# Kernel optimization log

Measured on AMD Instinct MI355X. Metric: run time of the kernel, lower is better.

Reference implementation:

```python
import jax, jax.numpy as jnp
import numpy as np
from jax import lax

N = 5000            # number of detections
FEAT = 1024         # last-layer feature dim; 1024 + 9 engineered feats = indim 1033
DIMS = [FEAT + 9, 1000, 600, 300, 150, 1]
IOU_THRESH = 0.5
EPS = 2.220446049250313e-16  # sys.float_info.epsilon


def setup_inputs() -> dict:
    key = jax.random.key(0)
    ks = jax.random.split(key, 8 + 3 * len(DIMS))
    H, W = 800.0, 1333.0
    cx = jax.random.uniform(ks[0], (N,), minval=0.0, maxval=W)
    cy = jax.random.uniform(ks[1], (N,), minval=0.0, maxval=H)
    bw = jax.random.uniform(ks[2], (N,), minval=20.0, maxval=250.0)
    bh = jax.random.uniform(ks[3], (N,), minval=20.0, maxval=250.0)
    x1 = jnp.clip(cx - bw / 2, 0.0, W - 2)
    y1 = jnp.clip(cy - bh / 2, 0.0, H - 2)
    x2 = jnp.clip(cx + bw / 2, x1 + 1, W)
    y2 = jnp.clip(cy + bh / 2, y1 + 1, H)
    inp = {
        'multi_bboxes': jnp.stack([x1, y1, x2, y2], axis=1),
        'cls_score': jax.random.uniform(ks[4], (N, 2)),
        'last_layer_feats': jax.random.normal(ks[5], (N, FEAT)),
        'img_shape': jnp.array([H, W], jnp.float32),
    }
    # PermEqui2_mean params: Gamma (weight+bias) and Lambda (weight only)
    ki = 6
    for i, (din, dout) in enumerate(zip(DIMS[:-1], DIMS[1:])):
        s = 1.0 / np.sqrt(din)
        inp[f'Wg{i+1}'] = jax.random.uniform(ks[ki], (dout, din), minval=-s, maxval=s); ki += 1
        inp[f'bg{i+1}'] = jax.random.uniform(ks[ki], (dout,), minval=-s, maxval=s); ki += 1
        inp[f'Wl{i+1}'] = jax.random.uniform(ks[ki], (dout, din), minval=-s, maxval=s); ki += 1
    return inp


def _greedy_cluster(ious, thresh):
    # Sequential greedy IoU clustering (NMS-like). assign[i] = index of cluster seed.
    n = ious.shape[0]

    def step(carry, inp):
        is_c, assign = carry
        j, row = inp
        seed = is_c[j]
        hit = row > thresh
        member = seed & hit & is_c
        assign = jnp.where(member, j, assign)
        is_c = is_c & ~(seed & hit)
        return (is_c, assign), None

    init = (jnp.ones(n, bool), jnp.zeros(n, jnp.int32))
    (_, assign), _ = lax.scan(step, init, (jnp.arange(n, dtype=jnp.int32), ious))
    return assign


def _forward(multi_bboxes, cls_score, last_layer_feats, img_shape, params):
    n = multi_bboxes.shape[0]
    scores = cls_score[:, 1]
    order = jnp.argsort(-scores)
    scores = scores[order]
    bboxes = multi_bboxes[order]
    feats = last_layer_feats[order]

    x1, y1, x2, y2 = bboxes[:, 0], bboxes[:, 1], bboxes[:, 2], bboxes[:, 3]
    # pairwise IoU with the +1 pixel convention from bbox_overlaps
    iw = jnp.clip(jnp.minimum(x2[:, None], x2[None, :]) - jnp.maximum(x1[:, None], x1[None, :]) + 1, 0)
    ih = jnp.clip(jnp.minimum(y2[:, None], y2[None, :]) - jnp.maximum(y1[:, None], y1[None, :]) + 1, 0)
    area = (x2 - x1 + 1) * (y2 - y1 + 1)
    overlap = iw * ih
    ious = overlap / (area[:, None] + area[None, :] - overlap)

    assign = _greedy_cluster(lax.stop_gradient(ious), IOU_THRESH)
    counts = jax.ops.segment_sum(jnp.ones(n, jnp.float32), assign, num_segments=n)
    cden = jnp.maximum(counts, 1.0)

    Himg, Wimg = img_shape[0], img_shape[1]
    # source double-normalizes: width = (x2/W - x1/W)/W, height = (y2/H - y1/H)/H
    width = (x2 / Wimg - x1 / Wimg) / Wimg
    height = (y2 / Himg - y1 / Himg) / Himg
    areaf = width * height
    ar = width / (height + EPS)
    x = jnp.concatenate([
        bboxes, feats,
        width[:, None], height[:, None], ar[:, None], areaf[:, None], scores[:, None],
    ], axis=1)  # [n, 1033]

    def perm_equi(x, Wg, bg, Wl):
        # xm = per-set mean; x*Gamma^T + b - (xm*Lambda^T), gathered back per box
        xm = jax.ops.segment_sum(x, assign, num_segments=n) / cden[:, None]
        return x @ Wg.T + bg - (xm @ Wl.T)[assign]

    for i in range(5):
        x = jax.nn.elu(perm_equi(x, params[f'Wg{i+1}'], params[f'bg{i+1}'], params[f'Wl{i+1}']))

    # source skips singleton sets (nonzero().squeeze() -> 0-dim): mask them out
    valid = counts[assign] >= 2.0
    return jnp.where(valid[:, None], x, 0.0)  # [n, 1] per-box set logits


def reference(multi_bboxes, cls_score, last_layer_feats, img_shape,
              Wg1, bg1, Wl1, Wg2, bg2, Wl2, Wg3, bg3, Wl3,
              Wg4, bg4, Wl4, Wg5, bg5, Wl5):
    params = {'Wg1': Wg1, 'bg1': bg1, 'Wl1': Wl1, 'Wg2': Wg2, 'bg2': bg2, 'Wl2': Wl2,
              'Wg3': Wg3, 'bg3': bg3, 'Wl3': Wl3, 'Wg4': Wg4, 'bg4': bg4, 'Wl4': Wl4,
              'Wg5': Wg5, 'bg5': bg5, 'Wl5': Wl5}
    return _forward(multi_bboxes, cls_score, last_layer_feats, img_shape, params)
```

## Files before the change

### kernel.cpp

```cpp
#include <hip/hip_runtime.h>
#include <cstdint>
#include <cstddef>

#define N_BOX 5000
#define NW    80
#define LDX   1040
#define LDZ   2048
#define LDYM  1000
#define LDW   1040
#define LDAB  2080
#define NCHUNK ((N_BOX + 63) / 64)
#define RT    ((N_BOX + 255) / 256)

typedef short bf16x8 __attribute__((ext_vector_type(8)));
typedef float f32x4v __attribute__((ext_vector_type(4)));
typedef unsigned short u16x8 __attribute__((ext_vector_type(8)));

__device__ __forceinline__ float fence_f(float x) { asm volatile("" : "+v"(x)); return x; }

__device__ __forceinline__ unsigned short f2bf(float x) {
    unsigned u = __builtin_bit_cast(unsigned, x);
    unsigned r = (u + 0x7FFFu + ((u >> 16) & 1u)) >> 16;
    return (unsigned short)r;
}
__device__ __forceinline__ float bf2f(unsigned short h) {
    unsigned u = ((unsigned)h) << 16;
    return __builtin_bit_cast(float, u);
}

__global__ void rank_partial_kernel(const float* __restrict__ cls, int* __restrict__ rank) {
    __shared__ float sj[256];
    int t = threadIdx.x;
    int jbase = blockIdx.y * 256;
    int jg = jbase + t;
    sj[t] = (jg < N_BOX) ? cls[2 * jg + 1] : 0.0f;
    __syncthreads();
    int i = blockIdx.x * 256 + t;
    if (i >= N_BOX) return;
    float si = cls[2 * i + 1];
    int jmax = (N_BOX - jbase < 256) ? (N_BOX - jbase) : 256;
    int r = 0;
    for (int k = 0; k < jmax; ++k) {
        float sjv = sj[k];
        int j = jbase + k;
        r += (sjv > si) || (sjv == si && j < i);
    }
    atomicAdd(&rank[i], r);
}

__global__ void rank_scatter_kernel(const int* __restrict__ rank, int* __restrict__ ord) {
    int i = blockIdx.x * blockDim.x + threadIdx.x;
    if (i < N_BOX) ord[rank[i]] = i;
}

__global__ void gather_kernel(const float* __restrict__ bb, const float* __restrict__ cls,
                              const float* __restrict__ feats, const float* __restrict__ img,
                              const int* __restrict__ ord,
                              float* __restrict__ X0, float* __restrict__ sb) {
    int r = blockIdx.x;
    int i = ord[r];
    float x1 = bb[4 * i + 0], y1 = bb[4 * i + 1], x2 = bb[4 * i + 2], y2 = bb[4 * i + 3];
    float H = img[0], W = img[1];
    float sc = cls[2 * i + 1];
    if (threadIdx.x == 0) {
        sb[0 * N_BOX + r] = x1;
        sb[1 * N_BOX + r] = y1;
        sb[2 * N_BOX + r] = x2;
        sb[3 * N_BOX + r] = y2;
        sb[4 * N_BOX + r] = (x2 - x1 + 1.0f) * (y2 - y1 + 1.0f);
        sb[5 * N_BOX + r] = sc;
    }
    float width  = (x2 / W - x1 / W) / W;
    float height = (y2 / H - y1 / H) / H;
    float ar     = width / (height + 2.220446049250313e-16f);
    float areaf  = width * height;
    float* row = X0 + (size_t)r * LDX;
    for (int o = threadIdx.x; o < LDX; o += blockDim.x) {
        float v;
        if (o < 4)          v = (o == 0) ? x1 : (o == 1) ? y1 : (o == 2) ? x2 : y2;
        else if (o < 1028)  v = feats[(size_t)i * 1024 + (o - 4)];
        else if (o == 1028) v = width;
        else if (o == 1029) v = height;
        else if (o == 1030) v = ar;
        else if (o == 1031) v = areaf;
        else if (o == 1032) v = sc;
        else                v = 0.0f;
        row[o] = v;
    }
}

__global__ void mask_kernel(const float* __restrict__ sb, unsigned long long* __restrict__ mask,
                            unsigned long long* __restrict__ diag) {
    int j = blockIdx.x;
    const float* X1 = sb;
    const float* Y1 = sb + N_BOX;
    const float* X2 = sb + 2 * N_BOX;
    const float* Y2 = sb + 3 * N_BOX;
    const float* AR = sb + 4 * N_BOX;
    float xj1 = X1[j], yj1 = Y1[j], xj2 = X2[j], yj2 = Y2[j], aj = AR[j];
    int lane = threadIdx.x & 63;
    int wave = threadIdx.x >> 6;
    int nwav = blockDim.x >> 6;
    int dw = j >> 6;
    for (int w = wave; w < NW; w += nwav) {
        int i = w * 64 + lane;
        bool pred = false;
        if (i < N_BOX) {
            float iw = fmaxf(fminf(xj2, X2[i]) - fmaxf(xj1, X1[i]) + 1.0f, 0.0f);
            float ih = fmaxf(fminf(yj2, Y2[i]) - fmaxf(yj1, Y1[i]) + 1.0f, 0.0f);
            float ov = fence_f(iw * ih);
            float denom = fence_f((aj + AR[i]) - ov);
            pred = (ov / denom) > 0.5f;
        }
        unsigned long long b = __ballot(pred);
        if (lane == 0) {
            mask[(size_t)j * NW + w] = b;
            if (w == dw) diag[j] = b;
        }
    }
}

__device__ __forceinline__ void nms_body(const unsigned long long* __restrict__ mask,
                                         const unsigned long long* __restrict__ diag,
                                         unsigned long long* __restrict__ keep,
                                         unsigned long long* supp,
                                         unsigned long long* keep_sh,
                                         unsigned long long* rem_sh,
                                         unsigned long long* kb_sh) {
    int tid = threadIdx.x;
    int l = tid & 63;
    int w = tid >> 6;
    if (tid < 80) supp[tid] = 0ULL;
    unsigned long long dg = 0ULL, dg_next = 0ULL;
    if (w == 0) dg = diag[l];
    __syncthreads();
    for (int c = 0; c < NCHUNK; ++c) {
        if (w == 0) {
            unsigned long long curv = supp[c];
            unsigned clo = __builtin_amdgcn_readfirstlane((unsigned)curv);
            unsigned chi = __builtin_amdgcn_readfirstlane((unsigned)(curv >> 32));
            unsigned long long cur = ((unsigned long long)chi << 32) | clo;
            int jmax = (N_BOX - c * 64 < 64) ? (N_BOX - c * 64) : 64;
            unsigned long long valid = (jmax >= 64) ? ~0ULL : ((1ULL << jmax) - 1ULL);
            unsigned long long rem = ~cur & valid;
            if (l == 0) *rem_sh = rem;
        }
        __syncthreads();
        unsigned long long rem0 = *rem_sh;
        unsigned long long a0 = 0, a1 = 0, a2 = 0, a3 = 0, a4 = 0;
        unsigned long long b0 = 0, b1 = 0, b2 = 0, b3 = 0, b4 = 0;
        unsigned mym = 0;
        int base = (w - 1) * 5;
        if (w > 0) {
            mym = (base < 64) ? (unsigned)((rem0 >> base) & 31ULL) : 0u;
            const unsigned long long* rowp = mask + (size_t)(c * 64 + base) * NW;
            if (mym & 1u)  { a0 = rowp[0 * NW + l]; b0 = (l < 16) ? rowp[0 * NW + 64 + l] : 0ULL; }
            if (mym & 2u)  { a1 = rowp[1 * NW + l]; b1 = (l < 16) ? rowp[1 * NW + 64 + l] : 0ULL; }
            if (mym & 4u)  { a2 = rowp[2 * NW + l]; b2 = (l < 16) ? rowp[2 * NW + 64 + l] : 0ULL; }
            if (mym & 8u)  { a3 = rowp[3 * NW + l]; b3 = (l < 16) ? rowp[3 * NW + 64 + l] : 0ULL; }
            if (mym & 16u) { a4 = rowp[4 * NW + l]; b4 = (l < 16) ? rowp[4 * NW + 64 + l] : 0ULL; }
        } else {
            if (c + 1 < NCHUNK) dg_next = diag[(size_t)(c + 1) * 64 + l];
            unsigned rlo = __builtin_amdgcn_readfirstlane((unsigned)rem0);
            unsigned rhi = __builtin_amdgcn_readfirstlane((unsigned)(rem0 >> 32));
            unsigned long long remS = ((unsigned long long)rhi << 32) | rlo;
            unsigned long long kb = 0ULL;
            while (remS) {
                int jj = __builtin_ctzll(remS);
                kb |= 1ULL << jj;
                unsigned dlo = __builtin_amdgcn_readlane((unsigned)dg, jj);
                unsigned dhi = __builtin_amdgcn_readlane((unsigned)(dg >> 32), jj);
                unsigned long long dj = ((unsigned long long)dhi << 32) | dlo;
                remS &= ~dj;
                remS &= ~(1ULL << jj);
            }
            if (l == 0) { *kb_sh = kb; keep_sh[c] = kb; }
        }
        __syncthreads();
        if (w > 0 && mym) {
            unsigned long long kb = *kb_sh;
            unsigned kw = ((unsigned)((kb >> base) & 31ULL)) & mym;
            if (kw & 1u)  { atomicOr(&supp[l], a0); if (l < 16) atomicOr(&supp[64 + l], b0); }
            if (kw & 2u)  { atomicOr(&supp[l], a1); if (l < 16) atomicOr(&supp[64 + l], b1); }
            if (kw & 4u)  { atomicOr(&supp[l], a2); if (l < 16) atomicOr(&supp[64 + l], b2); }
            if (kw & 8u)  { atomicOr(&supp[l], a3); if (l < 16) atomicOr(&supp[64 + l], b3); }
            if (kw & 16u) { atomicOr(&supp[l], a4); if (l < 16) atomicOr(&supp[64 + l], b4); }
        }
        if (w == 0) dg = dg_next;
        __syncthreads();
    }
    if (tid < NCHUNK) keep[tid] = keep_sh[tid];
}

__global__ __launch_bounds__(1024) void nms_scan_kernel(const unsigned long long* __restrict__ mask,
                                                        const unsigned long long* __restrict__ diag,
                                                        unsigned long long* __restrict__ keep) {
    __shared__ unsigned long long supp[80];
    __shared__ unsigned long long keep_sh[NCHUNK];
    __shared__ unsigned long long rem_sh;
    __shared__ unsigned long long kb_sh;
    nms_body(mask, diag, keep, supp, keep_sh, &rem_sh, &kb_sh);
}

__global__ __launch_bounds__(1024) void nms_gemm_fused(const unsigned long long* __restrict__ mask,
                                                       const unsigned long long* __restrict__ diag,
                                                       unsigned long long* __restrict__ keep,
                                                       const unsigned short* __restrict__ A2,
                                                       const unsigned short* __restrict__ B2,
                                                       float* __restrict__ C, int KT, int Nn,
                                                       int MTiles) {
    __shared__ __align__(16) unsigned short AsBuf[2 * 8192];
    __shared__ __align__(16) unsigned short BsBuf[2 * 8192];
    int tid = threadIdx.x;
    if (blockIdx.x == 0) {
        unsigned long long* supp    = (unsigned long long*)AsBuf;
        unsigned long long* keep_sh = supp + 80;
        unsigned long long* rem_sh  = keep_sh + NCHUNK;
        unsigned long long* kb_sh   = rem_sh + 1;
        nms_body(mask, diag, keep, supp, keep_sh, rem_sh, kb_sh);
        return;
    }
    int t = blockIdx.x - 1;
    size_t bm = (size_t)(t % MTiles) * 256;
    size_t bn = (size_t)(t / MTiles) * 256;
    int lane = tid & 63;
    int wavef = tid >> 6;
    int wr = wavef >> 2, wc = wavef & 3;

    f32x4v acc[4][4];
#pragma unroll
    for (int i = 0; i < 4; ++i)
#pragma unroll
        for (int j = 0; j < 4; ++j) acc[i][j] = (f32x4v){0.f, 0.f, 0.f, 0.f};

    const unsigned short* gA = A2 + (bm + wavef * 16 + (lane & 15)) * (size_t)LDAB + (lane >> 4) * 8;
    const unsigned short* gB = B2 + (bn + wavef * 16 + (lane & 15)) * (size_t)LDAB + (lane >> 4) * 8;
    unsigned ldsoff = (unsigned)((wavef * 64 + lane) * 16);

#define FSTAGE(T, BUF)                                                                             \
    {                                                                                              \
        size_t ko = (size_t)(T) * 32;                                                              \
        __builtin_amdgcn_global_load_lds(                                                          \
            (const __attribute__((address_space(1))) void*)(gA + ko),                              \
            (__attribute__((address_space(3))) void*)((char*)AsBuf + (BUF) * 16384 + ldsoff),      \
            16, 0, 0);                                                                             \
        __builtin_amdgcn_global_load_lds(                                                          \
            (const __attribute__((address_space(1))) void*)(gB + ko),                              \
            (__attribute__((address_space(3))) void*)((char*)BsBuf + (BUF) * 16384 + ldsoff),      \
            16, 0, 0);                                                                             \
    }

    FSTAGE(0, 0);
    for (int kt = 0; kt < KT; ++kt) {
        int cur = kt & 1;
        if (kt + 1 < KT) {
            FSTAGE(kt + 1, cur ^ 1);
            asm volatile("s_waitcnt vmcnt(2)" ::: "memory");
        } else {
            asm volatile("s_waitcnt vmcnt(0)" ::: "memory");
        }
        asm volatile("s_barrier" ::: "memory");
        bf16x8 af[4], bf[4];
#pragma unroll
        for (int f4 = 0; f4 < 4; ++f4) {
            af[f4] = *(const bf16x8*)((const char*)AsBuf + cur * 16384 + ((wr * 4 + f4) * 64 + lane) * 16);
            bf[f4] = *(const bf16x8*)((const char*)BsBuf + cur * 16384 + ((wc * 4 + f4) * 64 + lane) * 16);
        }
#pragma unroll
        for (int i = 0; i < 4; ++i)
#pragma unroll
            for (int j = 0; j < 4; ++j)
                acc[i][j] = __builtin_amdgcn_mfma_f32_16x16x32_bf16(af[i], bf[j], acc[i][j], 0, 0, 0);
        asm volatile("s_barrier" ::: "memory");
    }
#undef FSTAGE

#pragma unroll
    for (int i = 0; i < 4; ++i) {
        int r0 = (int)bm + wr * 64 + i * 16 + (lane >> 4) * 4;
#pragma unroll
        for (int j = 0; j < 4; ++j) {
            int col = (int)bn + wc * 64 + j * 16 + (lane & 15);
            if (col < Nn) {
#pragma unroll
                for (int e = 0; e < 4; ++e) {
                    int r = r0 + e;
                    if (r < N_BOX) C[(size_t)r * LDZ + col] = acc[i][j][e];
                }
            }
        }
    }
}

__global__ void zero_counts_kernel(int* __restrict__ counts) {
    int i = blockIdx.x * blockDim.x + threadIdx.x;
    if (i < N_BOX) counts[i] = 0;
}

__global__ void assign_kernel(const unsigned long long* __restrict__ mask,
                              const unsigned long long* __restrict__ keep,
                              int* __restrict__ assign, int* __restrict__ counts) {
    int i = blockIdx.x * blockDim.x + threadIdx.x;
    if (i >= N_BOX) return;
    for (int w = 0; w < NCHUNK; ++w) {
        unsigned long long m = mask[(size_t)i * NW + w] & keep[w];
        if (m) {
            int j = w * 64 + __builtin_ctzll(m);
            assign[i] = j;
            atomicAdd(&counts[j], 1);
            return;
        }
    }
}

__global__ __launch_bounds__(1024) void scan_kernel(const int* __restrict__ counts, int* __restrict__ offs) {
    __shared__ int part[1024];
    int t = threadIdx.x;
    int base = t * 5;
    int c[5];
    int s = 0;
#pragma unroll
    for (int k = 0; k < 5; ++k) {
        int idx = base + k;
        c[k] = (idx < N_BOX) ? counts[idx] : 0;
        s += c[k];
    }
    part[t] = s;
    __syncthreads();
    for (int d = 1; d < 1024; d <<= 1) {
        int v = part[t];
        int u = (t >= d) ? part[t - d] : 0;
        __syncthreads();
        part[t] = v + u;
        __syncthreads();
    }
    int run = (t > 0) ? part[t - 1] : 0;
#pragma unroll
    for (int k = 0; k < 5; ++k) {
        int idx = base + k;
        if (idx < N_BOX) offs[idx] = run;
        run += c[k];
    }
}

__global__ void rankscatter_kernel(const int* __restrict__ assign, const int* __restrict__ offs,
                                   int* __restrict__ members) {
    __shared__ int a[N_BOX];
    int tid = threadIdx.x;
    for (int t = tid; t < N_BOX; t += blockDim.x) a[t] = assign[t];
    __syncthreads();
    int i = blockIdx.x * blockDim.x + tid;
    if (i >= N_BOX) return;
    int ai = a[i];
    int r = 0;
    for (int k = 0; k < i; ++k) r += (a[k] == ai);
    members[offs[ai] + r] = i;
}

__global__ void xconv_kernel(const float* __restrict__ X, unsigned short* __restrict__ A2,
                             int K16eff, int colOff) {
    int r = blockIdx.x;
    unsigned short* dst = A2 + (size_t)r * LDAB;
    int K2 = 2 * K16eff;
    int nk8 = K2 >> 3;
    if (r >= N_BOX) {
        for (int k8 = threadIdx.x; k8 < nk8; k8 += blockDim.x) {
            u16x8 z;
#pragma unroll
            for (int j = 0; j < 8; ++j) z[j] = 0;
            *(u16x8*)(dst + (k8 << 3)) = z;
        }
        return;
    }
    const float* src = X + (size_t)r * LDX + colOff;
    for (int k8 = threadIdx.x; k8 < nk8; k8 += blockDim.x) {
        int kb = k8 << 3;
        bool lo = (kb >= K16eff);
        int ks = lo ? (kb - K16eff) : kb;
        u16x8 out;
#pragma unroll
        for (int j = 0; j < 8; ++j) {
            float x = src[ks + j];
            unsigned short ah = f2bf(x);
            out[j] = lo ? f2bf(x - bf2f(ah)) : ah;
        }
        *(u16x8*)(dst + kb) = out;
    }
}

__global__ void wconv_kernel(const float* __restrict__ Wg, const float* __restrict__ Wl,
                             unsigned short* __restrict__ B2, int dout, int din_src,
                             int din_eff, int colOff, int K16eff) {
    int n = blockIdx.x;
    unsigned short* dst = B2 + (size_t)n * LDAB;
    int K2 = 2 * K16eff;
    if (n >= 2 * dout) {
        for (int k = threadIdx.x; k < K2; k += blockDim.x) dst[k] = 0;
        return;
    }
    const float* src = (n < dout) ? (Wg + (size_t)n * din_src) : (Wl + (size_t)(n - dout) * din_src);
    for (int k = threadIdx.x; k < K2; k += blockDim.x) {
        int ks = (k >= K16eff) ? (k - K16eff) : k;
        float x = (ks < din_eff) ? src[colOff + ks] : 0.0f;
        dst[k] = f2bf(x);
    }
}

__global__ void e9_kernel(const float* __restrict__ X0, float* __restrict__ E9) {
    int r = blockIdx.x * blockDim.x + threadIdx.x;
    if (r >= 5120) return;
    const int cq[9] = {0, 1, 2, 3, 1028, 1029, 1030, 1031, 1032};
    float* dst = E9 + (size_t)r * 12;
#pragma unroll
    for (int q = 0; q < 9; ++q) dst[q] = (r < N_BOX) ? X0[(size_t)r * LDX + cq[q]] : 0.0f;
    dst[9] = dst[10] = dst[11] = 0.0f;
}
__global__ void w9_kernel(const float* __restrict__ Wg, const float* __restrict__ Wl,
                          float* __restrict__ W9, int NB) {
    int n = blockIdx.x * blockDim.x + threadIdx.x;
    if (n >= NB) return;
    const int cq[9] = {0, 1, 2, 3, 1028, 1029, 1030, 1031, 1032};
    float* dst = W9 + (size_t)n * 12;
    const float* src = (n < 1000) ? (Wg + (size_t)n * 1033)
                     : (n < 2000) ? (Wl + (size_t)(n - 1000) * 1033) : nullptr;
#pragma unroll
    for (int q = 0; q < 9; ++q) dst[q] = src ? src[cq[q]] : 0.0f;
    dst[9] = dst[10] = dst[11] = 0.0f;
}

__global__ void z9_patch_kernel(float* __restrict__ Z, const float* __restrict__ E9,
                                const float* __restrict__ W9, int Nn) {
    int r = blockIdx.x;
    float e[9];
#pragma unroll
    for (int q = 0; q < 9; ++q) e[q] = E9[(size_t)r * 12 + q];
    for (int o = threadIdx.x; o < Nn; o += blockDim.x) {
        const float* w = W9 + (size_t)o * 12;
        float s = 0.0f;
#pragma unroll
        for (int q = 0; q < 9; ++q) s += e[q] * w[q];
        Z[(size_t)r * LDZ + o] += s;
    }
}

__global__ __launch_bounds__(256, 4) void gemm_mfma(const unsigned short* __restrict__ A2,
                                                    const unsigned short* __restrict__ B2,
                                                    float* __restrict__ C, int KT, int Nn) {
    __shared__ unsigned short AsBuf[2 * 4096];
    __shared__ unsigned short BsBuf[2 * 4096];
    int tid = threadIdx.x;
    int lane = tid & 63;
    int wave = tid >> 6;
    int wr = wave >> 1, wc = wave & 1;
    size_t bm = (size_t)blockIdx.x * 128;
    size_t bn = (size_t)blockIdx.y * 128;

    f32x4v acc[4][4];
#pragma unroll
    for (int i = 0; i < 4; ++i)
#pragma unroll
        for (int j = 0; j < 4; ++j) acc[i][j] = (f32x4v){0.f, 0.f, 0.f, 0.f};

    const unsigned short* gA[2];
    const unsigned short* gB[2];
    unsigned ldsoff[2];
#pragma unroll
    for (int q = 0; q < 2; ++q) {
        int f = q * 4 + wave;
        int grow = f * 16 + (lane & 15);
        int gcol = (lane >> 4) * 8;
        gA[q] = A2 + (bm + grow) * (size_t)LDAB + gcol;
        gB[q] = B2 + (bn + grow) * (size_t)LDAB + gcol;
        ldsoff[q] = (unsigned)((f * 64 + lane) * 16);
    }

#define STAGE(T, BUF)                                                                              \
    {                                                                                              \
        size_t ko = (size_t)(T) * 32;                                                              \
        _Pragma("unroll") for (int q = 0; q < 2; ++q) {                                            \
            __builtin_amdgcn_global_load_lds(                                                      \
                (const __attribute__((address_space(1))) void*)(gA[q] + ko),                       \
                (__attribute__((address_space(3))) void*)((char*)AsBuf + (BUF) * 8192 + ldsoff[q]),\
                16, 0, 0);                                                                         \
            __builtin_amdgcn_global_load_lds(                                                      \
                (const __attribute__((address_space(1))) void*)(gB[q] + ko),                       \
                (__attribute__((address_space(3))) void*)((char*)BsBuf + (BUF) * 8192 + ldsoff[q]),\
                16, 0, 0);                                                                         \
        }                                                                                          \
    }

    STAGE(0, 0);
    for (int kt = 0; kt < KT; ++kt) {
        int cur = kt & 1;
        if (kt + 1 < KT) {
            STAGE(kt + 1, cur ^ 1);
            asm volatile("s_waitcnt vmcnt(4)" ::: "memory");
        } else {
            asm volatile("s_waitcnt vmcnt(0)" ::: "memory");
        }
        asm volatile("s_barrier" ::: "memory");
        bf16x8 af[4], bf[4];
#pragma unroll
        for (int f4 = 0; f4 < 4; ++f4) {
            af[f4] = *(const bf16x8*)((const char*)AsBuf + cur * 8192 + ((wr * 4 + f4) * 64 + lane) * 16);
            bf[f4] = *(const bf16x8*)((const char*)BsBuf + cur * 8192 + ((wc * 4 + f4) * 64 + lane) * 16);
        }
#pragma unroll
        for (int i = 0; i < 4; ++i)
#pragma unroll
            for (int j = 0; j < 4; ++j)
                acc[i][j] = __builtin_amdgcn_mfma_f32_16x16x32_bf16(af[i], bf[j], acc[i][j], 0, 0, 0);
        asm volatile("s_barrier" ::: "memory");
    }
#undef STAGE

#pragma unroll
    for (int i = 0; i < 4; ++i) {
        int r0 = (int)bm + wr * 64 + i * 16 + (lane >> 4) * 4;
#pragma unroll
        for (int j = 0; j < 4; ++j) {
            int col = (int)bn + wc * 64 + j * 16 + (lane & 15);
            if (col < Nn) {
#pragma unroll
                for (int e = 0; e < 4; ++e) {
                    int r = r0 + e;
                    if (r < N_BOX) C[(size_t)r * LDZ + col] = acc[i][j][e];
                }
            }
        }
    }
}

__global__ void wcat_kernel(const float* __restrict__ Wg, const float* __restrict__ Wl,
                            float* __restrict__ Wc, int dout, int din, int K16) {
    int row = blockIdx.x;
    const float* src = (row < dout) ? (Wg + (size_t)row * din) : (Wl + (size_t)(row - dout) * din);
    float* dst = Wc + (size_t)row * LDW;
    for (int k = threadIdx.x; k < K16; k += blockDim.x)
        dst[k] = (k < din) ? src[k] : 0.0f;
}

__global__ __launch_bounds__(256) void gemm_nt(const float* __restrict__ A, const float* __restrict__ B,
                                               float* __restrict__ C, int M, int Nn, int K16) {
    __shared__ float As[16][64];
    __shared__ float Bs[16][64];
    int bm = blockIdx.x * 64;
    int bn = blockIdx.y * 64;
    int tid = threadIdx.x;
    int row = tid & 63;
    int kq  = tid >> 6;
    int tx  = tid & 15;
    int ty  = tid >> 4;
    float acc[4][4] = {};
    for (int k0 = 0; k0 < K16; k0 += 16) {
        float4 av = make_float4(0.f, 0.f, 0.f, 0.f);
        float4 bv = make_float4(0.f, 0.f, 0.f, 0.f);
        if (bm + row < M)  av = *(const float4*)&A[(size_t)(bm + row) * LDX + k0 + kq * 4];
        if (bn + row < Nn) bv = *(const float4*)&B[(size_t)(bn + row) * LDW + k0 + kq * 4];
        __syncthreads();
        As[kq * 4 + 0][row] = av.x; As[kq * 4 + 1][row] = av.y;
        As[kq * 4 + 2][row] = av.z; As[kq * 4 + 3][row] = av.w;
        Bs[kq * 4 + 0][row] = bv.x; Bs[kq * 4 + 1][row] = bv.y;
        Bs[kq * 4 + 2][row] = bv.z; Bs[kq * 4 + 3][row] = bv.w;
        __syncthreads();
#pragma unroll
        for (int kk = 0; kk < 16; ++kk) {
            float4 a = *(const float4*)&As[kk][ty * 4];
            float4 b = *(const float4*)&Bs[kk][tx * 4];
            float aa[4] = {a.x, a.y, a.z, a.w};
            float bb[4] = {b.x, b.y, b.z, b.w};
#pragma unroll
            for (int i = 0; i < 4; ++i)
#pragma unroll
                for (int jx = 0; jx < 4; ++jx) acc[i][jx] += aa[i] * bb[jx];
        }
    }
#pragma unroll
    for (int i = 0; i < 4; ++i) {
        int r = bm + ty * 4 + i;
        if (r >= M) break;
#pragma unroll
        for (int jx = 0; jx < 4; ++jx) {
            int ccol = bn + tx * 4 + jx;
            if (ccol < Nn) C[(size_t)r * LDZ + ccol] = acc[i][jx];
        }
    }
}

__global__ void segmean_kernel(const float* __restrict__ Z, int dout,
                               const int* __restrict__ counts, const int* __restrict__ offs,
                               const int* __restrict__ members, float* __restrict__ ym) {
    int j = blockIdx.x;
    int cnt = counts[j];
    if (cnt == 0) return;
    int off = offs[j];
    float fc = (float)cnt;
    for (int o = threadIdx.x; o < dout; o += blockDim.x) {
        float s = 0.0f;
        for (int m = 0; m < cnt; ++m) {
            int i = members[off + m];
            s += Z[(size_t)i * LDZ + dout + o];
        }
        ym[(size_t)j * LDYM + o] = s / fc;
    }
}

__global__ void combine_kernel(const float* __restrict__ Z, const float* __restrict__ bg,
                               const float* __restrict__ ym, const int* __restrict__ assign,
                               float* __restrict__ Xout, int dout, int doutPad) {
    int r = blockIdx.x;
    int a = assign[r];
    float* dst = Xout + (size_t)r * LDX;
    for (int o = threadIdx.x; o < doutPad; o += blockDim.x) {
        float v = 0.0f;
        if (o < dout) {
            float z = Z[(size_t)r * LDZ + o] + bg[o] - ym[(size_t)a * LDYM + o];
            v = (z > 0.0f) ? z : expm1f(z);
        }
        dst[o] = v;
    }
}

__global__ void combine_fused_kernel(const float* __restrict__ Z, const float* __restrict__ bg,
                                     const float* __restrict__ ym, const int* __restrict__ assign,
                                     unsigned short* __restrict__ A2, int dout, int K16next) {
    int r = blockIdx.x;
    int a = assign[r];
    unsigned short* dst = A2 + (size_t)r * LDAB;
    for (int o = threadIdx.x; o < K16next; o += blockDim.x) {
        float v = 0.0f;
        if (o < dout) {
            float z = Z[(size_t)r * LDZ + o] + bg[o] - ym[(size_t)a * LDYM + o];
            v = (z > 0.0f) ? z : expm1f(z);
        }
        unsigned short hi = f2bf(v);
        dst[o] = hi;
        dst[K16next + o] = f2bf(v - bf2f(hi));
    }
}

__global__ void final_kernel(const float* __restrict__ X, const int* __restrict__ assign,
                             const int* __restrict__ counts, float* __restrict__ out) {
    int r = blockIdx.x * blockDim.x + threadIdx.x;
    if (r >= N_BOX) return;
    out[r] = (counts[assign[r]] >= 2) ? X[(size_t)r * LDX] : 0.0f;
}

extern "C" void kernel_launch(void* const* d_in, const int* in_sizes, int n_in,
                              void* d_out, int out_size, void* d_ws, size_t ws_size,
                              hipStream_t stream) {
    const float* bb    = (const float*)d_in[0];
    const float* cls   = (const float*)d_in[1];
    const float* feats = (const float*)d_in[2];
    const float* img   = (const float*)d_in[3];

    char* ws = (char*)d_ws;
    size_t off = 0;
    auto alloc = [&](size_t bytes) -> void* {
        void* p = ws + off;
        off += (bytes + 255) & ~(size_t)255;
        return p;
    };
    int*   ord     = (int*)alloc((size_t)N_BOX * 4);
    int*   rankb   = (int*)alloc((size_t)N_BOX * 4);
    float* sb      = (float*)alloc((size_t)6 * N_BOX * 4);
    int*   assign  = (int*)alloc((size_t)N_BOX * 4);
    int*   counts  = (int*)alloc((size_t)N_BOX * 4);
    int*   offsb   = (int*)alloc((size_t)N_BOX * 4);
    int*   members = (int*)alloc((size_t)N_BOX * 4);
    unsigned long long* mask = (unsigned long long*)alloc((size_t)(NCHUNK * 64) * NW * 8);
    unsigned long long* diag = (unsigned long long*)alloc((size_t)NCHUNK * 64 * 8);
    unsigned long long* keep = (unsigned long long*)alloc((size_t)NCHUNK * 8 + 1024);
    float* Xa = (float*)alloc((size_t)N_BOX * LDX * 4);
    float* Xb = (float*)alloc((size_t)N_BOX * LDX * 4);
    float* Z  = (float*)alloc((size_t)N_BOX * LDZ * 4);
    float* ym = (float*)alloc((size_t)N_BOX * LDYM * 4);
    float* Wc = (float*)alloc((size_t)2000 * LDW * 4);
    unsigned short* A2 = (unsigned short*)alloc((size_t)5120 * LDAB * 2);
    unsigned short* B2 = (unsigned short*)alloc((size_t)2048 * LDAB * 2);
    float* E9 = (float*)alloc((size_t)5120 * 12 * 4);
    float* W9 = (float*)alloc((size_t)2048 * 12 * 4);
    bool use_mfma = (off <= ws_size);

    hipMemsetAsync(rankb, 0, (size_t)N_BOX * 4, stream);
    rank_partial_kernel<<<dim3(RT, RT), dim3(256), 0, stream>>>(cls, rankb);
    rank_scatter_kernel<<<dim3(RT), dim3(256), 0, stream>>>(rankb, ord);
    gather_kernel<<<dim3(N_BOX), dim3(256), 0, stream>>>(bb, cls, feats, img, ord, Xa, sb);
    mask_kernel<<<dim3(N_BOX), dim3(256), 0, stream>>>(sb, mask, diag);
    zero_counts_kernel<<<dim3((N_BOX + 255) / 256), dim3(256), 0, stream>>>(counts);

    const int dins[5]  = {1033, 1000, 600, 300, 150};
    const int douts[5] = {1000, 600, 300, 150, 1};
    const int K16e[4]  = {1024, 1008, 608, 304};
    const int coff[4]  = {4, 0, 0, 0};
    const int dineff[4] = {1024, 1000, 600, 300};

    if (use_mfma) {
        e9_kernel<<<dim3(20), dim3(256), 0, stream>>>(Xa, E9);
        w9_kernel<<<dim3(8), dim3(256), 0, stream>>>((const float*)d_in[4], (const float*)d_in[6], W9, 2048);
        xconv_kernel<<<dim3(5120), dim3(256), 0, stream>>>(Xa, A2, K16e[0], coff[0]);
        wconv_kernel<<<dim3(2048), dim3(256), 0, stream>>>((const float*)d_in[4], (const float*)d_in[6],
                                                           B2, douts[0], dins[0], dineff[0], coff[0], K16e[0]);
        int KT0 = K16e[0] / 16;
        nms_gemm_fused<<<dim3(1 + 20 * 8), dim3(1024), 0, stream>>>(mask, diag, keep, A2, B2, Z,
                                                                    KT0, 2 * douts[0], 20);
        z9_patch_kernel<<<dim3(N_BOX), dim3(256), 0, stream>>>(Z, E9, W9, 2 * douts[0]);
    } else {
        nms_scan_kernel<<<dim3(1), dim3(1024), 0, stream>>>(mask, diag, keep);
    }

    assign_kernel<<<dim3((N_BOX + 255) / 256), dim3(256), 0, stream>>>(mask, keep, assign, counts);
    scan_kernel<<<dim3(1), dim3(1024), 0, stream>>>(counts, offsb);
    rankscatter_kernel<<<dim3((N_BOX + 255) / 256), dim3(256), 0, stream>>>(assign, offsb, members);

    for (int L = 0; L < 5; ++L) {
        const float* Wg = (const float*)d_in[4 + 3 * L];
        const float* bg = (const float*)d_in[5 + 3 * L];
        const float* Wl = (const float*)d_in[6 + 3 * L];
        int din = dins[L], dout = douts[L];
        int K16 = (din + 15) & ~15;
        int N2 = 2 * dout;
        int doutPad = (dout + 15) & ~15;
        float* Xin  = (L % 2 == 0) ? Xa : Xb;
        float* Xout = (L % 2 == 0) ? Xb : Xa;
        if (use_mfma && L < 4) {
            if (L > 0) {
                int KT = K16e[L] / 16;
                int Ntiles = (N2 + 127) >> 7;
                wconv_kernel<<<dim3(Ntiles * 128), dim3(256), 0, stream>>>(Wg, Wl, B2, dout, din,
                                                                           dineff[L], coff[L], K16e[L]);
                gemm_mfma<<<dim3(40, Ntiles), dim3(256), 0, stream>>>(A2, B2, Z, KT, N2);
            }
        } else {
            wcat_kernel<<<dim3(N2), dim3(256), 0, stream>>>(Wg, Wl, Wc, dout, din, K16);
            gemm_nt<<<dim3((N_BOX + 63) / 64, (N2 + 63) / 64), dim3(256), 0, stream>>>(Xin, Wc, Z, N_BOX, N2, K16);
        }
        segmean_kernel<<<dim3(N_BOX), dim3(256), 0, stream>>>(Z, dout, counts, offsb, members, ym);
        if (use_mfma && L < 3) {
            combine_fused_kernel<<<dim3(N_BOX), dim3(256), 0, stream>>>(Z, bg, ym, assign, A2,
                                                                        dout, K16e[L + 1]);
        } else {
            combine_kernel<<<dim3(N_BOX), dim3(256), 0, stream>>>(Z, bg, ym, assign, Xout, dout, doutPad);
        }
    }
    final_kernel<<<dim3((N_BOX + 255) / 256), dim3(256), 0, stream>>>(Xb, assign, counts, (float*)d_out);
}
```

Before: 572.9 us.

## Fuse setup kernels and hoist weight conversions into NMS/GEMM spare blocks

Result: slower. 664.6 us (+16.0%).

```diff
diff --git a/kernel.cpp b/kernel.cpp
--- a/kernel.cpp
+++ b/kernel.cpp
@@ -28,29 +28,28 @@
     return __builtin_bit_cast(float, u);
 }
 
-__global__ void rank_partial_kernel(const float* __restrict__ cls, int* __restrict__ rank) {
+__global__ __launch_bounds__(256) void rank_all_kernel(const float* __restrict__ cls, int* __restrict__ ord) {
     __shared__ float sj[256];
     int t = threadIdx.x;
-    int jbase = blockIdx.y * 256;
-    int jg = jbase + t;
-    sj[t] = (jg < N_BOX) ? cls[2 * jg + 1] : 0.0f;
-    __syncthreads();
     int i = blockIdx.x * 256 + t;
-    if (i >= N_BOX) return;
-    float si = cls[2 * i + 1];
-    int jmax = (N_BOX - jbase < 256) ? (N_BOX - jbase) : 256;
+    float si = (i < N_BOX) ? cls[2 * i + 1] : 0.0f;
     int r = 0;
-    for (int k = 0; k < jmax; ++k) {
-        float sjv = sj[k];
-        int j = jbase + k;
-        r += (sjv > si) || (sjv == si && j < i);
-    }
-    atomicAdd(&rank[i], r);
-}
-
-__global__ void rank_scatter_kernel(const int* __restrict__ rank, int* __restrict__ ord) {
-    int i = blockIdx.x * blockDim.x + threadIdx.x;
-    if (i < N_BOX) ord[rank[i]] = i;
+    for (int jt = 0; jt < RT; ++jt) {
+        int jbase = jt * 256;
+        int jg = jbase + t;
+        sj[t] = (jg < N_BOX) ? cls[2 * jg + 1] : 0.0f;
+        __syncthreads();
+        if (i < N_BOX) {
+            int jmax = (N_BOX - jbase < 256) ? (N_BOX - jbase) : 256;
+            for (int k = 0; k < jmax; ++k) {
+                float sjv = sj[k];
+                int j = jbase + k;
+                r += (sjv > si) || (sjv == si && j < i);
+            }
+        }
+        __syncthreads();
+    }
+    if (i < N_BOX) ord[r] = i;
 }
 
 __global__ void gather_kernel(const float* __restrict__ bb, const float* __restrict__ cls,
@@ -90,8 +89,9 @@
 }
 
 __global__ void mask_kernel(const float* __restrict__ sb, unsigned long long* __restrict__ mask,
-                            unsigned long long* __restrict__ diag) {
+                            unsigned long long* __restrict__ diag, int* __restrict__ counts) {
     int j = blockIdx.x;
+    if (threadIdx.x == 0) counts[j] = 0;
     const float* X1 = sb;
     const float* Y1 = sb + N_BOX;
     const float* X2 = sb + 2 * N_BOX;
@@ -202,17 +202,44 @@
     nms_body(mask, diag, keep, supp, keep_sh, &rem_sh, &kb_sh);
 }
 
+__device__ __forceinline__ void wconv_row(const float* __restrict__ Wg, const float* __restrict__ Wl,
+                                          unsigned short* __restrict__ B2, int n, int tid2,
+                                          int dout, int din, int K16) {
+    unsigned short* dst = B2 + (size_t)n * LDAB;
+    int K2 = 2 * K16;
+    if (n >= 2 * dout) {
+        for (int k = tid2; k < K2; k += 256) dst[k] = 0;
+        return;
+    }
+    const float* src = (n < dout) ? (Wg + (size_t)n * din) : (Wl + (size_t)(n - dout) * din);
+    for (int k = tid2; k < K2; k += 256) {
+        int ks = (k >= K16) ? (k - K16) : k;
+        float x = (ks < din) ? src[ks] : 0.0f;
+        dst[k] = f2bf(x);
+    }
+}
+
 __global__ __launch_bounds__(1024) void nms_gemm_fused(const unsigned long long* __restrict__ mask,
                                                        const unsigned long long* __restrict__ diag,
                                                        unsigned long long* __restrict__ keep,
                                                        const unsigned short* __restrict__ A2,
                                                        const unsigned short* __restrict__ B2,
                                                        float* __restrict__ C, int KT, int Nn,
-                                                       int MTiles) {
+                                                       int MTiles,
+                                                       const float* __restrict__ X0,
+                                                       float* __restrict__ E9, float* __restrict__ W9,
+                                                       const float* __restrict__ Wg1, const float* __restrict__ Wl1,
+                                                       const float* __restrict__ Wg0full, const float* __restrict__ Wl0full,
+                                                       unsigned short* __restrict__ B2_1,
+                                                       const float* __restrict__ Wg2, const float* __restrict__ Wl2,
+                                                       unsigned short* __restrict__ B2_2,
+                                                       const float* __restrict__ Wg3, const float* __restrict__ Wl3,
+                                                       unsigned short* __restrict__ B2_3) {
     __shared__ __align__(16) unsigned short AsBuf[2 * 8192];
     __shared__ __align__(16) unsigned short BsBuf[2 * 8192];
     int tid = threadIdx.x;
-    if (blockIdx.x == 0) {
+    int b = blockIdx.x;
+    if (b == 0) {
         unsigned long long* supp    = (unsigned long long*)AsBuf;
         unsigned long long* keep_sh = supp + 80;
         unsigned long long* rem_sh  = keep_sh + NCHUNK;
@@ -220,81 +247,158 @@
         nms_body(mask, diag, keep, supp, keep_sh, rem_sh, kb_sh);
         return;
     }
-    int t = blockIdx.x - 1;
-    size_t bm = (size_t)(t % MTiles) * 256;
-    size_t bn = (size_t)(t / MTiles) * 256;
-    int lane = tid & 63;
-    int wavef = tid >> 6;
-    int wr = wavef >> 2, wc = wavef & 3;
-
-    f32x4v acc[4][4];
-#pragma unroll
-    for (int i = 0; i < 4; ++i)
-#pragma unroll
-        for (int j = 0; j < 4; ++j) acc[i][j] = (f32x4v){0.f, 0.f, 0.f, 0.f};
-
-    const unsigned short* gA = A2 + (bm + wavef * 16 + (lane & 15)) * (size_t)LDAB + (lane >> 4) * 8;
-    const unsigned short* gB = B2 + (bn + wavef * 16 + (lane & 15)) * (size_t)LDAB + (lane >> 4) * 8;
-    unsigned ldsoff = (unsigned)((wavef * 64 + lane) * 16);
+    int NG = MTiles * 8;
+    if (b <= NG) {
+        int t = b - 1;
+        size_t bm = (size_t)(t % MTiles) * 256;
+        size_t bn = (size_t)(t / MTiles) * 256;
+        int lane = tid & 63;
+        int wavef = tid >> 6;
+        int wr = wavef >> 2, wc = wavef & 3;
+
+        f32x4v acc[4][4];
+#pragma unroll
+        for (int i = 0; i < 4; ++i)
+#pragma unroll
+            for (int j = 0; j < 4; ++j) acc[i][j] = (f32x4v){0.f, 0.f, 0.f, 0.f};
+
+        const unsigned short* gA = A2 + (bm + wavef * 16 + (lane & 15)) * (size_t)LDAB + (lane >> 4) * 8;
+        const unsigned short* gB = B2 + (bn + wavef * 16 + (lane & 15)) * (size_t)LDAB + (lane >> 4) * 8;
+        unsigned ldsoff = (unsigned)((wavef * 64 + lane) * 16);
 
 #define FSTAGE(T, BUF)                                                                             \
-    {                                                                                              \
-        size_t ko = (size_t)(T) * 32;                                                              \
-        __builtin_amdgcn_global_load_lds(                                                          \
-            (const __attribute__((address_space(1))) void*)(gA + ko),                              \
-            (__attribute__((address_space(3))) void*)((char*)AsBuf + (BUF) * 16384 + ldsoff),      \
-            16, 0, 0);                                                                             \
-        __builtin_amdgcn_global_load_lds(                                                          \
-            (const __attribute__((address_space(1))) void*)(gB + ko),                              \
-            (__attribute__((address_space(3))) void*)((char*)BsBuf + (BUF) * 16384 + ldsoff),      \
-            16, 0, 0);                                                                             \
-    }
-
-    FSTAGE(0, 0);
-    for (int kt = 0; kt < KT; ++kt) {
-        int cur = kt & 1;
-        if (kt + 1 < KT) {
-            FSTAGE(kt + 1, cur ^ 1);
-            asm volatile("s_waitcnt vmcnt(2)" ::: "memory");
-        } else {
-            asm volatile("s_waitcnt vmcnt(0)" ::: "memory");
-        }
-        asm volatile("s_barrier" ::: "memory");
-        bf16x8 af[4], bf[4];
-#pragma unroll
-        for (int f4 = 0; f4 < 4; ++f4) {
-            af[f4] = *(const bf16x8*)((const char*)AsBuf + cur * 16384 + ((wr * 4 + f4) * 64 + lane) * 16);
-            bf[f4] = *(const bf16x8*)((const char*)BsBuf + cur * 16384 + ((wc * 4 + f4) * 64 + lane) * 16);
-        }
-#pragma unroll
-        for (int i = 0; i < 4; ++i)
-#pragma unroll
-            for (int j = 0; j < 4; ++j)
-                acc[i][j] = __builtin_amdgcn_mfma_f32_16x16x32_bf16(af[i], bf[j], acc[i][j], 0, 0, 0);
-        asm volatile("s_barrier" ::: "memory");
-    }
+        {                                                                                          \
+            size_t ko = (size_t)(T) * 32;                                                          \
+            __builtin_amdgcn_global_load_lds(                                                      \
+                (const __attribute__((address_space(1))) void*)(gA + ko),                          \
+                (__attribute__((address_space(3))) void*)((char*)AsBuf + (BUF) * 16384 + ldsoff),  \
+                16, 0, 0);                                                                         \
+            __builtin_amdgcn_global_load_lds(                                                      \
+                (const __attribute__((address_space(1))) void*)(gB + ko),                          \
+                (__attribute__((address_space(3))) void*)((char*)BsBuf + (BUF) * 16384 + ldsoff),  \
+                16, 0, 0);                                                                         \
+        }
+
+        FSTAGE(0, 0);
+        for (int kt = 0; kt < KT; ++kt) {
+            int cur = kt & 1;
+            if (kt + 1 < KT) {
+                FSTAGE(kt + 1, cur ^ 1);
+                asm volatile("s_waitcnt vmcnt(2)" ::: "memory");
+            } else {
+                asm volatile("s_waitcnt vmcnt(0)" ::: "memory");
+            }
+            asm volatile("s_barrier" ::: "memory");
+            bf16x8 af[4], bf[4];
+#pragma unroll
+            for (int f4 = 0; f4 < 4; ++f4) {
+                af[f4] = *(const bf16x8*)((const char*)AsBuf + cur * 16384 + ((wr * 4 + f4) * 64 + lane) * 16);
+                bf[f4] = *(const bf16x8*)((const char*)BsBuf + cur * 16384 + ((wc * 4 + f4) * 64 + lane) * 16);
+            }
+#pragma unroll
+            for (int i = 0; i < 4; ++i)
+#pragma unroll
+                for (int j = 0; j < 4; ++j)
+                    acc[i][j] = __builtin_amdgcn_mfma_f32_16x16x32_bf16(af[i], bf[j], acc[i][j], 0, 0, 0);
+            asm volatile("s_barrier" ::: "memory");
+        }
 #undef FSTAGE
 
 #pragma unroll
-    for (int i = 0; i < 4; ++i) {
-        int r0 = (int)bm + wr * 64 + i * 16 + (lane >> 4) * 4;
-#pragma unroll
-        for (int j = 0; j < 4; ++j) {
-            int col = (int)bn + wc * 64 + j * 16 + (lane & 15);
-            if (col < Nn) {
-#pragma unroll
-                for (int e = 0; e < 4; ++e) {
-                    int r = r0 + e;
-                    if (r < N_BOX) C[(size_t)r * LDZ + col] = acc[i][j][e];
+        for (int i = 0; i < 4; ++i) {
+            int r0 = (int)bm + wr * 64 + i * 16 + (lane >> 4) * 4;
+#pragma unroll
+            for (int j = 0; j < 4; ++j) {
+                int col = (int)bn + wc * 64 + j * 16 + (lane & 15);
+                if (col < Nn) {
+#pragma unroll
+                    for (int e = 0; e < 4; ++e) {
+                        int r = r0 + e;
+                        if (r < N_BOX) C[(size_t)r * LDZ + col] = acc[i][j][e];
+                    }
                 }
             }
         }
-    }
-}
-
-__global__ void zero_counts_kernel(int* __restrict__ counts) {
-    int i = blockIdx.x * blockDim.x + threadIdx.x;
-    if (i < N_BOX) counts[i] = 0;
+        return;
+    }
+    int rb = b - 1 - NG;
+    const int cq[9] = {0, 1, 2, 3, 1028, 1029, 1030, 1031, 1032};
+    if (rb < 5) {
+        int r = rb * 1024 + tid;
+        if (r < 5120) {
+            float* dst = E9 + (size_t)r * 12;
+#pragma unroll
+            for (int q = 0; q < 9; ++q) dst[q] = (r < N_BOX) ? X0[(size_t)r * LDX + cq[q]] : 0.0f;
+            dst[9] = dst[10] = dst[11] = 0.0f;
+        }
+        return;
+    }
+    rb -= 5;
+    if (rb < 2) {
+        int n = rb * 1024 + tid;
+        if (n < 2048) {
+            float* dst = W9 + (size_t)n * 12;
+            const float* src = (n < 1000) ? (Wg0full + (size_t)n * 1033)
+                             : (n < 2000) ? (Wl0full + (size_t)(n - 1000) * 1033) : nullptr;
+#pragma unroll
+            for (int q = 0; q < 9; ++q) dst[q] = src ? src[cq[q]] : 0.0f;
+            dst[9] = dst[10] = dst[11] = 0.0f;
+        }
+        return;
+    }
+    rb -= 2;
+    int rowl = tid >> 8;
+    int tid2 = tid & 255;
+    if (rb < 320) {
+        int n = rb * 4 + rowl;
+        if (n < 1280) wconv_row(Wg1, Wl1, B2_1, n, tid2, 600, 1000, 1008);
+        return;
+    }
+    rb -= 320;
+    if (rb < 160) {
+        int n = rb * 4 + rowl;
+        if (n < 640) wconv_row(Wg2, Wl2, B2_2, n, tid2, 300, 600, 608);
+        return;
+    }
+    rb -= 160;
+    {
+        int n = rb * 4 + rowl;
+        if (n < 384) wconv_row(Wg3, Wl3, B2_3, n, tid2, 150, 300, 304);
+        return;
+    }
+}
+
+__global__ void z9_assign_kernel(float* __restrict__ Z, const float* __restrict__ E9,
+                                 const float* __restrict__ W9, int Nn,
+                                 const unsigned long long* __restrict__ mask,
+                                 const unsigned long long* __restrict__ keep,
+                                 int* __restrict__ assign, int* __restrict__ counts) {
+    int b = blockIdx.x;
+    if (b < N_BOX) {
+        int r = b;
+        float e[9];
+#pragma unroll
+        for (int q = 0; q < 9; ++q) e[q] = E9[(size_t)r * 12 + q];
+        for (int o = threadIdx.x; o < Nn; o += blockDim.x) {
+            const float* w = W9 + (size_t)o * 12;
+            float s = 0.0f;
+#pragma unroll
+            for (int q = 0; q < 9; ++q) s += e[q] * w[q];
+            Z[(size_t)r * LDZ + o] += s;
+        }
+        return;
+    }
+    int i = (b - N_BOX) * 256 + threadIdx.x;
+    if (i >= N_BOX) return;
+    for (int w = 0; w < NCHUNK; ++w) {
+        unsigned long long m = mask[(size_t)i * NW + w] & keep[w];
+        if (m) {
+            int j = w * 64 + __builtin_ctzll(m);
+            assign[i] = j;
+            atomicAdd(&counts[j], 1);
+            return;
+        }
+    }
 }
 
 __global__ void assign_kernel(const unsigned long long* __restrict__ mask,
@@ -403,43 +507,6 @@
         int ks = (k >= K16eff) ? (k - K16eff) : k;
         float x = (ks < din_eff) ? src[colOff + ks] : 0.0f;
         dst[k] = f2bf(x);
-    }
-}
-
-__global__ void e9_kernel(const float* __restrict__ X0, float* __restrict__ E9) {
-    int r = blockIdx.x * blockDim.x + threadIdx.x;
-    if (r >= 5120) return;
-    const int cq[9] = {0, 1, 2, 3, 1028, 1029, 1030, 1031, 1032};
-    float* dst = E9 + (size_t)r * 12;
-#pragma unroll
-    for (int q = 0; q < 9; ++q) dst[q] = (r < N_BOX) ? X0[(size_t)r * LDX + cq[q]] : 0.0f;
-    dst[9] = dst[10] = dst[11] = 0.0f;
-}
-__global__ void w9_kernel(const float* __restrict__ Wg, const float* __restrict__ Wl,
-                          float* __restrict__ W9, int NB) {
-    int n = blockIdx.x * blockDim.x + threadIdx.x;
-    if (n >= NB) return;
-    const int cq[9] = {0, 1, 2, 3, 1028, 1029, 1030, 1031, 1032};
-    float* dst = W9 + (size_t)n * 12;
-    const float* src = (n < 1000) ? (Wg + (size_t)n * 1033)
-                     : (n < 2000) ? (Wl + (size_t)(n - 1000) * 1033) : nullptr;
-#pragma unroll
-    for (int q = 0; q < 9; ++q) dst[q] = src ? src[cq[q]] : 0.0f;
-    dst[9] = dst[10] = dst[11] = 0.0f;
-}
-
-__global__ void z9_patch_kernel(float* __restrict__ Z, const float* __restrict__ E9,
-                                const float* __restrict__ W9, int Nn) {
-    int r = blockIdx.x;
-    float e[9];
-#pragma unroll
-    for (int q = 0; q < 9; ++q) e[q] = E9[(size_t)r * 12 + q];
-    for (int o = threadIdx.x; o < Nn; o += blockDim.x) {
-        const float* w = W9 + (size_t)o * 12;
-        float s = 0.0f;
-#pragma unroll
-        for (int q = 0; q < 9; ++q) s += e[q] * w[q];
-        Z[(size_t)r * LDZ + o] += s;
     }
 }
 
@@ -662,7 +729,6 @@
         return p;
     };
     int*   ord     = (int*)alloc((size_t)N_BOX * 4);
-    int*   rankb   = (int*)alloc((size_t)N_BOX * 4);
     float* sb      = (float*)alloc((size_t)6 * N_BOX * 4);
     int*   assign  = (int*)alloc((size_t)N_BOX * 4);
     int*   counts  = (int*)alloc((size_t)N_BOX * 4);
@@ -676,42 +742,48 @@
     float* Z  = (float*)alloc((size_t)N_BOX * LDZ * 4);
     float* ym = (float*)alloc((size_t)N_BOX * LDYM * 4);
     float* Wc = (float*)alloc((size_t)2000 * LDW * 4);
-    unsigned short* A2 = (unsigned short*)alloc((size_t)5120 * LDAB * 2);
-    unsigned short* B2 = (unsigned short*)alloc((size_t)2048 * LDAB * 2);
+    unsigned short* A2   = (unsigned short*)alloc((size_t)5120 * LDAB * 2);
+    unsigned short* B2_0 = (unsigned short*)alloc((size_t)2048 * LDAB * 2);
+    unsigned short* B2_1 = (unsigned short*)alloc((size_t)1280 * LDAB * 2);
+    unsigned short* B2_2 = (unsigned short*)alloc((size_t)640 * LDAB * 2);
+    unsigned short* B2_3 = (unsigned short*)alloc((size_t)384 * LDAB * 2);
     float* E9 = (float*)alloc((size_t)5120 * 12 * 4);
     float* W9 = (float*)alloc((size_t)2048 * 12 * 4);
     bool use_mfma = (off <= ws_size);
 
-    hipMemsetAsync(rankb, 0, (size_t)N_BOX * 4, stream);
-    rank_partial_kernel<<<dim3(RT, RT), dim3(256), 0, stream>>>(cls, rankb);
-    rank_scatter_kernel<<<dim3(RT), dim3(256), 0, stream>>>(rankb, ord);
+    rank_all_kernel<<<dim3(RT), dim3(256), 0, stream>>>(cls, ord);
     gather_kernel<<<dim3(N_BOX), dim3(256), 0, stream>>>(bb, cls, feats, img, ord, Xa, sb);
-    mask_kernel<<<dim3(N_BOX), dim3(256), 0, stream>>>(sb, mask, diag);
-    zero_counts_kernel<<<dim3((N_BOX + 255) / 256), dim3(256), 0, stream>>>(counts);
+    mask_kernel<<<dim3(N_BOX), dim3(256), 0, stream>>>(sb, mask, diag, counts);
 
     const int dins[5]  = {1033, 1000, 600, 300, 150};
     const int douts[5] = {1000, 600, 300, 150, 1};
     const int K16e[4]  = {1024, 1008, 608, 304};
     const int coff[4]  = {4, 0, 0, 0};
     const int dineff[4] = {1024, 1000, 600, 300};
+    unsigned short* B2L[4] = {B2_0, B2_1, B2_2, B2_3};
 
     if (use_mfma) {
-        e9_kernel<<<dim3(20), dim3(256), 0, stream>>>(Xa, E9);
-        w9_kernel<<<dim3(8), dim3(256), 0, stream>>>((const float*)d_in[4], (const float*)d_in[6], W9, 2048);
         xconv_kernel<<<dim3(5120), dim3(256), 0, stream>>>(Xa, A2, K16e[0], coff[0]);
         wconv_kernel<<<dim3(2048), dim3(256), 0, stream>>>((const float*)d_in[4], (const float*)d_in[6],
-                                                           B2, douts[0], dins[0], dineff[0], coff[0], K16e[0]);
+                                                           B2_0, douts[0], dins[0], dineff[0], coff[0], K16e[0]);
         int KT0 = K16e[0] / 16;
-        nms_gemm_fused<<<dim3(1 + 20 * 8), dim3(1024), 0, stream>>>(mask, diag, keep, A2, B2, Z,
-                                                                    KT0, 2 * douts[0], 20);
-        z9_patch_kernel<<<dim3(N_BOX), dim3(256), 0, stream>>>(Z, E9, W9, 2 * douts[0]);
+        nms_gemm_fused<<<dim3(744), dim3(1024), 0, stream>>>(
+            mask, diag, keep, A2, B2_0, Z, KT0, 2 * douts[0], 20,
+            Xa, E9, W9,
+            (const float*)d_in[7], (const float*)d_in[9],
+            (const float*)d_in[4], (const float*)d_in[6],
+            B2_1,
+            (const float*)d_in[10], (const float*)d_in[12], B2_2,
+            (const float*)d_in[13], (const float*)d_in[15], B2_3);
+        z9_assign_kernel<<<dim3(N_BOX + RT), dim3(256), 0, stream>>>(Z, E9, W9, 2 * douts[0],
+                                                                     mask, keep, assign, counts);
     } else {
         nms_scan_kernel<<<dim3(1), dim3(1024), 0, stream>>>(mask, diag, keep);
-    }
-
-    assign_kernel<<<dim3((N_BOX + 255) / 256), dim3(256), 0, stream>>>(mask, keep, assign, counts);
+        assign_kernel<<<dim3(RT), dim3(256), 0, stream>>>(mask, keep, assign, counts);
+    }
+
     scan_kernel<<<dim3(1), dim3(1024), 0, stream>>>(counts, offsb);
-    rankscatter_kernel<<<dim3((N_BOX + 255) / 256), dim3(256), 0, stream>>>(assign, offsb, members);
+    rankscatter_kernel<<<dim3(RT), dim3(256), 0, stream>>>(assign, offsb, members);
 
     for (int L = 0; L < 5; ++L) {
         const float* Wg = (const float*)d_in[4 + 3 * L];
@@ -727,9 +799,7 @@
             if (L > 0) {
                 int KT = K16e[L] / 16;
                 int Ntiles = (N2 + 127) >> 7;
-                wconv_kernel<<<dim3(Ntiles * 128), dim3(256), 0, stream>>>(Wg, Wl, B2, dout, din,
-                                                                           dineff[L], coff[L], K16e[L]);
-                gemm_mfma<<<dim3(40, Ntiles), dim3(256), 0, stream>>>(A2, B2, Z, KT, N2);
+                gemm_mfma<<<dim3(40, Ntiles), dim3(256), 0, stream>>>(A2, B2L[L], Z, KT, N2);
             }
         } else {
             wcat_kernel<<<dim3(N2), dim3(256), 0, stream>>>(Wg, Wl, Wc, dout, din, K16);
@@ -743,5 +813,5 @@
             combine_kernel<<<dim3(N_BOX), dim3(256), 0, stream>>>(Z, bg, ym, assign, Xout, dout, doutPad);
         }
     }
-    final_kernel<<<dim3((N_BOX + 255) / 256), dim3(256), 0, stream>>>(Xb, assign, counts, (float*)d_out);
-}
+    final_kernel<<<dim3(RT), dim3(256), 0, stream>>>(Xb, assign, counts, (float*)d_out);
+}
```
